# Optimization experiments

Hardware: AMD Instinct MI355X
Metric: run time of the kernel (lower is better)

## Reference

```python
import jax, jax.numpy as jnp
import numpy as np

ANCHOR_SIZES = [64.0, 128.0, 256.0]
ANCHOR_RATIOS = [0.5, 1.0, 2.0]
STD_SCALING = 1.0
RPN_STRIDE = 16
PRE_NMS_TOP_N = 3000
POST_NMS_TOP_N = 300
NMS_IOU_THRES = 0.7


def make_anchors():
    # ratios are sqrt'd as in the original __init__; anchors stored as (w, h)
    rs = [np.sqrt(r) for r in ANCHOR_RATIOS]
    a = [[s * r, s / r] for s in ANCHOR_SIZES for r in rs]
    return np.array(a, dtype=np.float32)  # [A, 2]


def setup_inputs() -> dict:
    key = jax.random.key(0)
    k1, k2 = jax.random.split(key)
    B, A, H, W = 4, 9, 34, 60
    rpn_scores = jax.random.uniform(k1, (B, A, H, W), dtype=jnp.float32)
    rpn_deltas = jax.random.normal(k2, (B, 4 * A, H, W), dtype=jnp.float32)
    input_image = jnp.zeros((B, 3, 544, 960), dtype=jnp.float32)  # only shape is used
    return {"rpn_scores": rpn_scores, "rpn_deltas": rpn_deltas, "input_image": input_image}


def _pairwise_iou(boxes):
    # boxes: [N, 4] in (x1, y1, x2, y2)
    x1, y1, x2, y2 = boxes[:, 0], boxes[:, 1], boxes[:, 2], boxes[:, 3]
    area = (x2 - x1) * (y2 - y1)
    iw = jnp.maximum(jnp.minimum(x2[:, None], x2[None, :]) - jnp.maximum(x1[:, None], x1[None, :]), 0.0)
    ih = jnp.maximum(jnp.minimum(y2[:, None], y2[None, :]) - jnp.maximum(y1[:, None], y1[None, :]), 0.0)
    inter = iw * ih
    union = area[:, None] + area[None, :] - inter
    return inter / jnp.maximum(union, 1e-8)


def _nms_single(boxes, probs):
    # pre-NMS top-N by score, then greedy IoU suppression, then post-NMS top-N (zero-padded)
    scores_k, idx = jax.lax.top_k(probs, PRE_NMS_TOP_N)
    boxes_k = boxes[idx]                                 # [pre_N, 4]
    iou = _pairwise_iou(boxes_k)                         # [pre_N, pre_N]

    def body(active, i):
        keep_i = active[i]
        sup = (iou[i] > NMS_IOU_THRES) & keep_i
        sup = sup.at[i].set(False)
        return active & ~sup, keep_i

    _, keep = jax.lax.scan(body, jnp.ones((PRE_NMS_TOP_N,), bool), jnp.arange(PRE_NMS_TOP_N))
    sel = jnp.where(keep, scores_k, -jnp.inf)
    _, kidx = jax.lax.top_k(sel, POST_NMS_TOP_N)
    valid = keep[kidx]
    return jnp.where(valid[:, None], boxes_k[kidx], 0.0)  # [post_N, 4]


def _forward(rpn_scores, rpn_deltas, input_image):
    B, A, H, W = rpn_scores.shape
    img_h = jnp.float32(input_image.shape[2])
    img_w = jnp.float32(input_image.shape[3])
    # NCHW -> NHWC -> [B,H,W,A,4]; channel layout is anchor-major, coord-minor
    deltas = (rpn_deltas * (1.0 / STD_SCALING)).transpose(0, 2, 3, 1).reshape(B, H, W, A, 4)
    ancs = jnp.asarray(make_anchors())                   # [A, 2] (w, h)
    aw, ah = ancs[:, 0], ancs[:, 1]
    # anchor centers on the RPN grid, at input-image scale
    cx = jnp.broadcast_to(((jnp.arange(W, dtype=jnp.float32) + 0.5) * RPN_STRIDE)[None, :, None], (H, W, A))
    cy = jnp.broadcast_to(((jnp.arange(H, dtype=jnp.float32) + 0.5) * RPN_STRIDE)[:, None, None], (H, W, A))
    tx, ty, tw, th = deltas[..., 0], deltas[..., 1], deltas[..., 2], deltas[..., 3]
    ctr_x = cx + tx * aw
    ctr_y = cy + ty * ah
    w1 = jnp.exp(tw) * aw
    h1 = jnp.exp(th) * ah
    x1 = ctr_x - 0.5 * w1
    y1 = ctr_y - 0.5 * h1
    x2 = x1 + w1
    y2 = y1 + h1
    x1 = jnp.clip(x1, 0.0, img_w - 1.0)
    x2 = jnp.clip(x2, 0.0, img_w - 1.0)
    y1 = jnp.clip(y1, 0.0, img_h - 1.0)
    y2 = jnp.clip(y2, 0.0, img_h - 1.0)
    boxes = jnp.stack([x1, y1, x2, y2], axis=-1)          # [B,H,W,A,4]
    boxes = boxes.transpose(0, 3, 1, 2, 4).reshape(B, -1, 4)  # [B, A*H*W, 4] (matches score layout)
    probs = rpn_scores.reshape(B, -1)
    return jax.vmap(_nms_single)(boxes, probs)            # [B, post_N, 4]


def reference(rpn_scores, rpn_deltas, input_image):
    return _forward(rpn_scores, rpn_deltas, input_image)
```

## Files before the change

kernel.cpp:

```cpp
#include <hip/hip_runtime.h>
#include <stdint.h>

typedef uint32_t u32;
typedef uint64_t u64;

#define NB 4
#define NA 9
#define NH 34
#define NW 60
#define HW (NH*NW)
#define NBOX (NA*HW)
#define PRE_NMS 3000
#define POST_NMS 300
#define NBUCKET 4096
#define SEGCAP 4096
#define NTH 1024
#define PER 18
#define CORNER 512
#define CW 8
#define SUB 16
#define NCH (CORNER/SUB)

__device__ __constant__ float c_aw[9] = {
  45.254833995939045f, 64.0f,  90.50966799187808f,
  90.50966799187808f,  128.0f, 181.01933598375617f,
  181.01933598375617f, 256.0f, 362.03867196751233f };
__device__ __constant__ float c_ah[9] = {
  90.50966799187808f,  64.0f,  45.254833995939045f,
  181.01933598375617f, 128.0f, 90.50966799187808f,
  362.03867196751233f, 256.0f, 181.01933598375617f };

__device__ __forceinline__ u64 readlane64(u64 v, int lane) {
  u32 lo = __builtin_amdgcn_readlane((u32)(v & 0xffffffffull), lane);
  u32 hi = __builtin_amdgcn_readlane((u32)(v >> 32), lane);
  return ((u64)hi << 32) | lo;
}

__device__ __forceinline__ float4 decode_box(const float* __restrict__ dl, int idx) {
  int a = idx / HW;
  int r = idx - a * HW;
  int h = r / NW;
  int w = r - h * NW;
  const float* dp = dl + (4 * a) * HW + r;
  float tx = dp[0];
  float ty = dp[HW];
  float tw = dp[2 * HW];
  float th = dp[3 * HW];
  float aw = c_aw[a], ah = c_ah[a];
  float ctr_x = ((float)w + 0.5f) * 16.0f + tx * aw;
  float ctr_y = ((float)h + 0.5f) * 16.0f + ty * ah;
  float w1 = expf(tw) * aw;
  float h1 = expf(th) * ah;
  float x1 = ctr_x - 0.5f * w1;
  float y1 = ctr_y - 0.5f * h1;
  float x2 = x1 + w1;
  float y2 = y1 + h1;
  x1 = fminf(fmaxf(x1, 0.0f), 959.0f);
  x2 = fminf(fmaxf(x2, 0.0f), 959.0f);
  y1 = fminf(fmaxf(y1, 0.0f), 543.0f);
  y2 = fminf(fmaxf(y2, 0.0f), 543.0f);
  return make_float4(x1, y1, x2, y2);
}

__global__ void __launch_bounds__(NTH)
topk_rank_decode_kernel(const float* __restrict__ scores,
                        const float* __restrict__ deltas,
                        float4* __restrict__ boxes_ws)
{
  __shared__ u32 s_base[NBUCKET];
  __shared__ u32 s_cnt[NBUCKET];
  __shared__ u64 s_keys[SEGCAP];
  __shared__ u32 s_sfx[NTH];

  const int tid = threadIdx.x;
  const int b   = blockIdx.x;
  const float* sc = scores + b * NBOX;

  for (int t = tid; t < NBUCKET; t += NTH) s_cnt[t] = 0;
  __syncthreads();

  for (int m = 0; m < PER; ++m) {
    int i = tid + m * NTH;
    if (i < NBOX) {
      float s = sc[i];
      int bk = (int)(s * (float)NBUCKET);
      bk = bk < 0 ? 0 : (bk > NBUCKET - 1 ? NBUCKET - 1 : bk);
      atomicAdd(&s_cnt[bk], 1u);
    }
  }
  __syncthreads();

  u32 h0 = s_cnt[4*tid], h1 = s_cnt[4*tid+1], h2 = s_cnt[4*tid+2], h3 = s_cnt[4*tid+3];
  s_sfx[tid] = h0 + h1 + h2 + h3;
  __syncthreads();
  for (int d = 1; d < NTH; d <<= 1) {
    u32 v = (tid + d < NTH) ? s_sfx[tid + d] : 0u;
    __syncthreads();
    s_sfx[tid] += v;
    __syncthreads();
  }

  {
    u32 Gn = (tid < NTH - 1) ? s_sfx[tid + 1] : 0u;
    s_base[4*tid+3] = Gn;
    s_base[4*tid+2] = Gn + h3;
    s_base[4*tid+1] = Gn + h3 + h2;
    s_base[4*tid+0] = Gn + h3 + h2 + h1;
  }
  __syncthreads();

  for (int t = tid; t < NBUCKET; t += NTH) s_cnt[t] = 0;
  for (int t = tid; t < SEGCAP; t += NTH) s_keys[t] = 0ull;
  __syncthreads();

  for (int m = 0; m < PER; ++m) {
    int i = tid + m * NTH;
    if (i < NBOX) {
      float s = sc[i];
      int bk = (int)(s * (float)NBUCKET);
      bk = bk < 0 ? 0 : (bk > NBUCKET - 1 ? NBUCKET - 1 : bk);
      u32 base = s_base[bk];
      if (base < PRE_NMS) {
        u32 loc = atomicAdd(&s_cnt[bk], 1u);
        u32 pos = base + loc;
        if (pos < SEGCAP) {
          u64 key = ((u64)__float_as_uint(s) << 32) | (u32)(~(u32)i);
          s_keys[pos] = key;
        }
      }
    }
  }
  __syncthreads();

  const float* dl = deltas + b * (4 * NA * HW);
  for (int m = 0; m < SEGCAP / NTH; ++m) {
    int p = tid + m * NTH;
    u64 key = s_keys[p];
    float s = __uint_as_float((u32)(key >> 32));
    int bk = (int)(s * (float)NBUCKET);
    bk = bk < 0 ? 0 : (bk > NBUCKET - 1 ? NBUCKET - 1 : bk);
    u32 base = s_base[bk];
    u32 cnt  = s_cnt[bk];
    u32 local = 0;
    for (u32 q = base; q < base + cnt; ++q)
      local += (s_keys[q] > key) ? 1u : 0u;
    u32 R = base + local;
    if (key != 0ull && R < PRE_NMS) {
      int idx = (int)(~(u32)key);
      boxes_ws[b * PRE_NMS + R] = decode_box(dl, idx);
    }
  }
}

__global__ void __launch_bounds__(256)
mask_corner_kernel(const float4* __restrict__ boxes_ws, u64* __restrict__ masks2)
{
  const int wq = blockIdx.x;
  const int rh = blockIdx.y;
  const int b  = blockIdx.z;
  const int tid = threadIdx.x;
  __shared__ float4 s_cb[128];
  __shared__ float  s_ca[128];
  if (tid < 128) {
    int j = 128 * wq + tid;
    float4 v = boxes_ws[b * PRE_NMS + j];
    s_cb[tid] = v;
    s_ca[tid] = (v.z - v.x) * (v.w - v.y);
  }
  __syncthreads();
  int row = rh * 256 + tid;
  float4 r = boxes_ws[b * PRE_NMS + row];
  float ra = (r.z - r.x) * (r.w - r.y);
  #pragma unroll
  for (int wl = 0; wl < 2; ++wl) {
    u64 word = 0;
    #pragma unroll
    for (int k = 0; k < 64; ++k) {
      float4 cb = s_cb[wl * 64 + k];
      float iw = fminf(r.z, cb.z) - fmaxf(r.x, cb.x);
      float ih = fminf(r.w, cb.w) - fmaxf(r.y, cb.y);
      iw = fmaxf(iw, 0.0f);
      ih = fmaxf(ih, 0.0f);
      float inter = iw * ih;
      float uni = ra + s_ca[wl * 64 + k] - inter;
      word |= ((u64)(inter > 0.7f * fmaxf(uni, 1e-8f))) << k;
    }
    masks2[((size_t)b * CORNER + row) * CW + (2 * wq + wl)] = word;
  }
}

__global__ void __launch_bounds__(256)
nms_reduce_kernel(const float4* __restrict__ boxes_ws,
                  const u64* __restrict__ masks2,
                  float* __restrict__ out)
{
  const int b = blockIdx.x;
  const int tid = threadIdx.x;
  __shared__ __align__(16) u64 s_corner[CORNER * CW];
  __shared__ u32 s_kept[POST_NMS];
  __shared__ u32 s_nk;

  {
    const ulonglong2* src = (const ulonglong2*)(masks2 + (size_t)b * CORNER * CW);
    ulonglong2* dst = (ulonglong2*)s_corner;
    #pragma unroll
    for (int k = 0; k < (CORNER * CW / 2) / 256; ++k)
      dst[tid + k * 256] = src[tid + k * 256];
  }
  __syncthreads();

  if (tid < 64) {
    const int lane = tid;
    const int wl8 = lane & 7;
    u64 removed = 0ull;
    int nk = 0;
    bool done = false;

    u64 D = (lane < 16) ? s_corner[lane * CW + 0] : 0ull;

    for (int j = 0; j < NCH && !done; ++j) {
      const int base = j * SUB;
      const int w0 = j >> 2;
      const int sh = (j & 3) * 16;
      const int jn = j + 1;
      u64 Dn = (jn < NCH && lane < 16)
                 ? s_corner[(jn * SUB + lane) * CW + (jn >> 2)] : 0ull;
      u64 remw = readlane64(removed, w0);
      u32 a = (u32)((~remw >> sh) & 0xFFFFull);
      u64 supw = 0ull;
      u32 keepm = 0;
      while (a) {
        int k = __ffs(a) - 1;
        a &= a - 1u;
        if (!((supw >> (sh + k)) & 1ull)) {
          keepm |= 1u << k;
          if (lane == 0) s_kept[nk] = (u32)(base + k);
          ++nk;
          if (nk >= POST_NMS) { done = true; break; }
          supw |= readlane64(D, k);
        }
      }
      if (!done) {
        #pragma unroll
        for (int k = 0; k < SUB; ++k) {
          u64 rw = s_corner[(base + k) * CW + wl8];
          if ((keepm >> k) & 1u) removed |= rw;
        }
      }
      D = Dn;
    }

    if (nk < POST_NMS) {
      float4 kb[5];
      float  ka[5];
      #pragma unroll
      for (int s = 0; s < 5; ++s) {
        int t = s * 64 + lane;
        float4 v = make_float4(0.f, 0.f, 0.f, 0.f);
        if (t < nk) v = boxes_ws[b * PRE_NMS + s_kept[t]];
        kb[s] = v;
        ka[s] = (v.z - v.x) * (v.w - v.y);
      }
      for (int i = CORNER; i < PRE_NMS; ++i) {
        if (nk >= POST_NMS) break;
        float4 c = boxes_ws[b * PRE_NMS + i];
        float carea = (c.z - c.x) * (c.w - c.y);
        bool over = false;
        #pragma unroll
        for (int s = 0; s < 5; ++s) {
          if (s * 64 < nk) {
            if (s * 64 + lane < nk) {
              float iw = fminf(kb[s].z, c.z) - fmaxf(kb[s].x, c.x);
              float ih = fminf(kb[s].w, c.w) - fmaxf(kb[s].y, c.y);
              iw = fmaxf(iw, 0.0f);
              ih = fmaxf(ih, 0.0f);
              float inter = iw * ih;
              float uni = ka[s] + carea - inter;
              over = over || (inter > 0.7f * fmaxf(uni, 1e-8f));
            }
          }
        }
        if (__ballot((int)over) == 0ull) {
          int s = nk >> 6, l = nk & 63;
          #pragma unroll
          for (int q = 0; q < 5; ++q)
            if (q == s && lane == l) { kb[q] = c; ka[q] = carea; }
          if (lane == 0) s_kept[nk] = (u32)i;
          ++nk;
        }
      }
    }
    if (lane == 0) s_nk = (u32)nk;
  }
  __syncthreads();

  u32 fnk = s_nk;
  float4* outv = (float4*)out;
  for (int t = tid; t < POST_NMS; t += 256) {
    float4 v = make_float4(0.f, 0.f, 0.f, 0.f);
    if ((u32)t < fnk) v = boxes_ws[b * PRE_NMS + s_kept[t]];
    outv[b * POST_NMS + t] = v;
  }
}

__global__ void __launch_bounds__(NTH)
rpn_proposal_mono(const float* __restrict__ scores,
                  const float* __restrict__ deltas,
                  float* __restrict__ out)
{
  __shared__ __align__(16) char smem[16384 + 32768 + 4096];
  u32* s_hist = (u32*)smem;
  u64* s_cand = (u64*)(smem + 16384);
  u32* s_sfx  = (u32*)(smem + 16384 + 32768);
  float4* s_box = (float4*)smem;
  __shared__ u32 s_kept[POST_NMS];
  __shared__ u32 s_meta[4];

  const int tid = threadIdx.x;
  const int b   = blockIdx.x;
  const float* sc = scores + b * NBOX;

  for (int t = tid; t < NBUCKET; t += NTH) s_hist[t] = 0;
  if (tid < 4) s_meta[tid] = 0;
  __syncthreads();
  for (int m = 0; m < PER; ++m) {
    int i = tid + m * NTH;
    if (i < NBOX) {
      float s = sc[i];
      int bk = (int)(s * (float)NBUCKET);
      bk = bk < 0 ? 0 : (bk > NBUCKET - 1 ? NBUCKET - 1 : bk);
      atomicAdd(&s_hist[bk], 1u);
    }
  }
  __syncthreads();
  {
    u32 g = s_hist[4*tid] + s_hist[4*tid+1] + s_hist[4*tid+2] + s_hist[4*tid+3];
    s_sfx[tid] = g;
  }
  __syncthreads();
  for (int d = 1; d < NTH; d <<= 1) {
    u32 v = (tid + d < NTH) ? s_sfx[tid + d] : 0u;
    __syncthreads();
    s_sfx[tid] += v;
    __syncthreads();
  }
  {
    u32 sg  = s_sfx[tid];
    u32 sgn = (tid < NTH - 1) ? s_sfx[tid + 1] : 0u;
    if (sg >= PRE_NMS && sgn < PRE_NMS) {
      u32 c = sgn;
      for (int t = 4 * tid + 3; t >= 4 * tid; --t) {
        c += s_hist[t];
        if (c >= PRE_NMS) { s_meta[0] = (u32)t; s_meta[1] = c; break; }
      }
    }
  }
  __syncthreads();
  const u32 T = s_meta[0];
  for (int m = 0; m < PER; ++m) {
    int i = tid + m * NTH;
    if (i < NBOX) {
      float s = sc[i];
      int bk = (int)(s * (float)NBUCKET);
      bk = bk < 0 ? 0 : (bk > NBUCKET - 1 ? NBUCKET - 1 : bk);
      if ((u32)bk >= T) {
        u32 pos = atomicAdd(&s_meta[2], 1u);
        if (pos < SEGCAP) {
          u64 key = ((u64)__float_as_uint(s) << 32) | (u32)(~(u32)i);
          s_cand[pos] = key;
        }
      }
    }
  }
  __syncthreads();
  {
    u32 C = s_meta[2]; if (C > SEGCAP) C = SEGCAP;
    for (u32 p = C + tid; p < SEGCAP; p += NTH) s_cand[p] = 0ull;
  }
  for (int kk = 2; kk <= SEGCAP; kk <<= 1) {
    for (int j = kk >> 1; j > 0; j >>= 1) {
      __syncthreads();
      #pragma unroll
      for (int m = 0; m < 2; ++m) {
        int t = tid + m * NTH;
        int i = ((t & ~(j - 1)) << 1) | (t & (j - 1));
        int p = i | j;
        u64 a  = s_cand[i];
        u64 bb = s_cand[p];
        bool desc = (i & kk) == 0;
        bool sw = desc ? (a < bb) : (a > bb);
        if (sw) { s_cand[i] = bb; s_cand[p] = a; }
      }
    }
  }
  __syncthreads();
  const float* dl = deltas + b * (4 * NA * HW);
  float4 bx[3];
  #pragma unroll
  for (int m = 0; m < 3; ++m) {
    int k = tid + m * NTH;
    if (k < PRE_NMS) {
      u64 key = s_cand[k];
      bx[m] = decode_box(dl, (int)(~(u32)key));
    }
  }
  __syncthreads();
  #pragma unroll
  for (int m = 0; m < 3; ++m) {
    int k = tid + m * NTH;
    if (k < PRE_NMS) s_box[k] = bx[m];
  }
  __syncthreads();
  if (tid < 64) {
    const int lane = tid;
    float4 kb[5];
    float  ka[5];
    int nk = 0;
    for (int i = 0; i < PRE_NMS; ++i) {
      if (nk >= POST_NMS) break;
      float4 c = s_box[i];
      float carea = (c.z - c.x) * (c.w - c.y);
      bool over = false;
      #pragma unroll
      for (int s = 0; s < 5; ++s) {
        if (s * 64 < nk) {
          if (s * 64 + lane < nk) {
            float iw = fminf(kb[s].z, c.z) - fmaxf(kb[s].x, c.x);
            float ih = fminf(kb[s].w, c.w) - fmaxf(kb[s].y, c.y);
            iw = fmaxf(iw, 0.0f);
            ih = fmaxf(ih, 0.0f);
            float inter = iw * ih;
            float uni = ka[s] + carea - inter;
            over = over || (inter > 0.7f * fmaxf(uni, 1e-8f));
          }
        }
      }
      if (__ballot((int)over) == 0ull) {
        int s = nk >> 6, l = nk & 63;
        #pragma unroll
        for (int q = 0; q < 5; ++q)
          if (q == s && lane == l) { kb[q] = c; ka[q] = carea; }
        if (lane == 0) s_kept[nk] = (u32)i;
        ++nk;
      }
    }
    if (lane == 0) s_meta[3] = (u32)nk;
  }
  __syncthreads();
  if (tid < POST_NMS) {
    u32 nk = s_meta[3];
    float4 v = make_float4(0.0f, 0.0f, 0.0f, 0.0f);
    if ((u32)tid < nk) v = s_box[s_kept[tid]];
    ((float4*)out)[b * POST_NMS + tid] = v;
  }
}

extern "C" void kernel_launch(void* const* d_in, const int* in_sizes, int n_in,
                              void* d_out, int out_size, void* d_ws, size_t ws_size,
                              hipStream_t stream) {
  const float* scores = (const float*)d_in[0];
  const float* deltas = (const float*)d_in[1];
  (void)in_sizes; (void)n_in; (void)out_size;

  const size_t mask_off   = 196608;
  const size_t mask_bytes = (size_t)NB * CORNER * CW * sizeof(u64);
  const size_t need       = mask_off + mask_bytes;

  if (ws_size >= need) {
    float4* boxes_ws = (float4*)d_ws;
    u64*    masks2   = (u64*)((char*)d_ws + mask_off);
    topk_rank_decode_kernel<<<dim3(NB), dim3(NTH), 0, stream>>>(scores, deltas, boxes_ws);
    mask_corner_kernel<<<dim3(4, 2, NB), dim3(256), 0, stream>>>(boxes_ws, masks2);
    nms_reduce_kernel<<<dim3(NB), dim3(256), 0, stream>>>(boxes_ws, masks2, (float*)d_out);
  } else {
    rpn_proposal_mono<<<dim3(NB), dim3(NTH), 0, stream>>>(scores, deltas, (float*)d_out);
  }
}
```

Measured before the change: 150.1 us.

## Expand precomputed IoU mask to 1536 candidates with register-resident row-chain NMS

The precomputed suppression bitmask grows from the top 512 to the top 1536 candidates (24 words per row), and the corner mask kernel now launches more blocks, one 64-column word each. The reduce kernel becomes a single wavefront. For each 64-box chunk it ORs each lane's mask row against the accumulated keep masks held in registers, uses a ballot to find unsuppressed boxes, resolves the intra-chunk greedy order with readlane, and prefetches the next chunk's rows from global memory. This moves more of the greedy scan off the slow serial per-candidate IoU fallback. The cost is a larger mask computation and workspace, plus heavy register use.

```diff
diff --git a/kernel.cpp b/kernel.cpp
--- a/kernel.cpp
+++ b/kernel.cpp
@@ -16,10 +16,9 @@
 #define SEGCAP 4096
 #define NTH 1024
 #define PER 18
-#define CORNER 512
-#define CW 8
-#define SUB 16
-#define NCH (CORNER/SUB)
+#define NCAND 1536
+#define MW 24
+#define NCHK 24
 
 __device__ __constant__ float c_aw[9] = {
   45.254833995939045f, 64.0f,  90.50966799187808f,
@@ -156,149 +155,177 @@
 mask_corner_kernel(const float4* __restrict__ boxes_ws, u64* __restrict__ masks2)
 {
   const int wq = blockIdx.x;
-  const int rh = blockIdx.y;
+  const int rb = blockIdx.y;
   const int b  = blockIdx.z;
   const int tid = threadIdx.x;
-  __shared__ float4 s_cb[128];
-  __shared__ float  s_ca[128];
-  if (tid < 128) {
-    int j = 128 * wq + tid;
+  __shared__ float4 s_cb[64];
+  __shared__ float  s_ca[64];
+  if (tid < 64) {
+    int j = wq * 64 + tid;
     float4 v = boxes_ws[b * PRE_NMS + j];
     s_cb[tid] = v;
     s_ca[tid] = (v.z - v.x) * (v.w - v.y);
   }
   __syncthreads();
-  int row = rh * 256 + tid;
+  int row = rb * 256 + tid;
   float4 r = boxes_ws[b * PRE_NMS + row];
   float ra = (r.z - r.x) * (r.w - r.y);
+  u64 word = 0;
   #pragma unroll
-  for (int wl = 0; wl < 2; ++wl) {
-    u64 word = 0;
-    #pragma unroll
-    for (int k = 0; k < 64; ++k) {
-      float4 cb = s_cb[wl * 64 + k];
-      float iw = fminf(r.z, cb.z) - fmaxf(r.x, cb.x);
-      float ih = fminf(r.w, cb.w) - fmaxf(r.y, cb.y);
-      iw = fmaxf(iw, 0.0f);
-      ih = fmaxf(ih, 0.0f);
-      float inter = iw * ih;
-      float uni = ra + s_ca[wl * 64 + k] - inter;
-      word |= ((u64)(inter > 0.7f * fmaxf(uni, 1e-8f))) << k;
-    }
-    masks2[((size_t)b * CORNER + row) * CW + (2 * wq + wl)] = word;
-  }
-}
-
-__global__ void __launch_bounds__(256)
+  for (int k = 0; k < 64; ++k) {
+    float4 cb = s_cb[k];
+    float iw = fminf(r.z, cb.z) - fmaxf(r.x, cb.x);
+    float ih = fminf(r.w, cb.w) - fmaxf(r.y, cb.y);
+    iw = fmaxf(iw, 0.0f);
+    ih = fmaxf(ih, 0.0f);
+    float inter = iw * ih;
+    float uni = ra + s_ca[k] - inter;
+    word |= ((u64)(inter > 0.7f * fmaxf(uni, 1e-8f))) << k;
+  }
+  masks2[((size_t)b * NCAND + row) * MW + wq] = word;
+}
+
+__global__ void __launch_bounds__(64)
 nms_reduce_kernel(const float4* __restrict__ boxes_ws,
                   const u64* __restrict__ masks2,
                   float* __restrict__ out)
 {
   const int b = blockIdx.x;
-  const int tid = threadIdx.x;
-  __shared__ __align__(16) u64 s_corner[CORNER * CW];
+  const int lane = threadIdx.x;
   __shared__ u32 s_kept[POST_NMS];
-  __shared__ u32 s_nk;
-
-  {
-    const ulonglong2* src = (const ulonglong2*)(masks2 + (size_t)b * CORNER * CW);
-    ulonglong2* dst = (ulonglong2*)s_corner;
+
+  const u64* mrow = masks2 + (size_t)b * NCAND * MW;
+  int nk = 0;
+  bool done = false;
+
+  ulonglong2 cur0, cur1, cur2, cur3, cur4, cur5, cur6, cur7, cur8, cur9, cur10, cur11;
+  ulonglong2 nxt0, nxt1, nxt2, nxt3, nxt4, nxt5, nxt6, nxt7, nxt8, nxt9, nxt10, nxt11;
+  ulonglong2 km0, km1, km2, km3, km4, km5, km6, km7, km8, km9, km10, km11;
+  km0 = km1 = km2 = km3 = km4 = km5 = km6 = km7 = km8 = km9 = km10 = km11
+      = make_ulonglong2(0ull, 0ull);
+
+#define LOADCUR(C) { const ulonglong2* p_ = (const ulonglong2*)mrow + ((size_t)((C)*64 + lane)) * (MW/2); \
+  cur0=p_[0]; cur1=p_[1]; cur2=p_[2]; cur3=p_[3]; cur4=p_[4]; cur5=p_[5]; \
+  cur6=p_[6]; cur7=p_[7]; cur8=p_[8]; cur9=p_[9]; cur10=p_[10]; cur11=p_[11]; }
+#define PREF(C) { const ulonglong2* p_ = (const ulonglong2*)mrow + ((size_t)((C)*64 + lane)) * (MW/2); \
+  nxt0=p_[0]; nxt1=p_[1]; nxt2=p_[2]; nxt3=p_[3]; nxt4=p_[4]; nxt5=p_[5]; \
+  nxt6=p_[6]; nxt7=p_[7]; nxt8=p_[8]; nxt9=p_[9]; nxt10=p_[10]; nxt11=p_[11]; }
+#define ROLL { cur0=nxt0; cur1=nxt1; cur2=nxt2; cur3=nxt3; cur4=nxt4; cur5=nxt5; \
+  cur6=nxt6; cur7=nxt7; cur8=nxt8; cur9=nxt9; cur10=nxt10; cur11=nxt11; }
+#define DO_CHUNK(C, DW, KM) {                                            \
+    u64 sA_ = (cur0.x & km0.x) | (cur0.y & km0.y)                        \
+            | (cur1.x & km1.x) | (cur1.y & km1.y)                        \
+            | (cur2.x & km2.x) | (cur2.y & km2.y)                        \
+            | (cur3.x & km3.x) | (cur3.y & km3.y)                        \
+            | (cur4.x & km4.x) | (cur4.y & km4.y)                        \
+            | (cur5.x & km5.x) | (cur5.y & km5.y)                        \
+            | (cur6.x & km6.x) | (cur6.y & km6.y)                        \
+            | (cur7.x & km7.x) | (cur7.y & km7.y)                        \
+            | (cur8.x & km8.x) | (cur8.y & km8.y)                        \
+            | (cur9.x & km9.x) | (cur9.y & km9.y)                        \
+            | (cur10.x & km10.x) | (cur10.y & km10.y)                    \
+            | (cur11.x & km11.x) | (cur11.y & km11.y);                   \
+    u64 a_ = __ballot(sA_ == 0ull);                                      \
+    u64 supw_ = 0ull, keepm_ = 0ull;                                     \
+    while (a_) {                                                         \
+      int k_ = __ffsll((unsigned long long)a_) - 1;                      \
+      a_ &= a_ - 1ull;                                                   \
+      if (!((supw_ >> k_) & 1ull)) {                                     \
+        keepm_ |= 1ull << k_;                                            \
+        ++nk;                                                            \
+        if (nk >= POST_NMS) break;                                       \
+        supw_ |= readlane64(DW, k_);                                     \
+      }                                                                  \
+    }                                                                    \
+    if (lane == 0) {                                                     \
+      u64 km_ = keepm_;                                                  \
+      int c2_ = nk - __popcll((unsigned long long)keepm_);               \
+      while (km_) {                                                      \
+        int k_ = __ffsll((unsigned long long)km_) - 1;                   \
+        km_ &= km_ - 1ull;                                               \
+        s_kept[c2_++] = (u32)((C) * 64 + k_);                            \
+      }                                                                  \
+    }                                                                    \
+    KM |= keepm_;                                                        \
+    done = (nk >= POST_NMS);                                             \
+  }
+
+  LOADCUR(0); PREF(1);
+  DO_CHUNK( 0, cur0.x,  km0.x ); if (done) goto chain_done; ROLL; PREF(2);
+  DO_CHUNK( 1, cur0.y,  km0.y ); if (done) goto chain_done; ROLL; PREF(3);
+  DO_CHUNK( 2, cur1.x,  km1.x ); if (done) goto chain_done; ROLL; PREF(4);
+  DO_CHUNK( 3, cur1.y,  km1.y ); if (done) goto chain_done; ROLL; PREF(5);
+  DO_CHUNK( 4, cur2.x,  km2.x ); if (done) goto chain_done; ROLL; PREF(6);
+  DO_CHUNK( 5, cur2.y,  km2.y ); if (done) goto chain_done; ROLL; PREF(7);
+  DO_CHUNK( 6, cur3.x,  km3.x ); if (done) goto chain_done; ROLL; PREF(8);
+  DO_CHUNK( 7, cur3.y,  km3.y ); if (done) goto chain_done; ROLL; PREF(9);
+  DO_CHUNK( 8, cur4.x,  km4.x ); if (done) goto chain_done; ROLL; PREF(10);
+  DO_CHUNK( 9, cur4.y,  km4.y ); if (done) goto chain_done; ROLL; PREF(11);
+  DO_CHUNK(10, cur5.x,  km5.x ); if (done) goto chain_done; ROLL; PREF(12);
+  DO_CHUNK(11, cur5.y,  km5.y ); if (done) goto chain_done; ROLL; PREF(13);
+  DO_CHUNK(12, cur6.x,  km6.x ); if (done) goto chain_done; ROLL; PREF(14);
+  DO_CHUNK(13, cur6.y,  km6.y ); if (done) goto chain_done; ROLL; PREF(15);
+  DO_CHUNK(14, cur7.x,  km7.x ); if (done) goto chain_done; ROLL; PREF(16);
+  DO_CHUNK(15, cur7.y,  km7.y ); if (done) goto chain_done; ROLL; PREF(17);
+  DO_CHUNK(16, cur8.x,  km8.x ); if (done) goto chain_done; ROLL; PREF(18);
+  DO_CHUNK(17, cur8.y,  km8.y ); if (done) goto chain_done; ROLL; PREF(19);
+  DO_CHUNK(18, cur9.x,  km9.x ); if (done) goto chain_done; ROLL; PREF(20);
+  DO_CHUNK(19, cur9.y,  km9.y ); if (done) goto chain_done; ROLL; PREF(21);
+  DO_CHUNK(20, cur10.x, km10.x); if (done) goto chain_done; ROLL; PREF(22);
+  DO_CHUNK(21, cur10.y, km10.y); if (done) goto chain_done; ROLL; PREF(23);
+  DO_CHUNK(22, cur11.x, km11.x); if (done) goto chain_done; ROLL;
+  DO_CHUNK(23, cur11.y, km11.y);
+chain_done: ;
+#undef DO_CHUNK
+#undef ROLL
+#undef PREF
+#undef LOADCUR
+
+  if (nk < POST_NMS) {
+    float4 kb[5];
+    float  ka[5];
     #pragma unroll
-    for (int k = 0; k < (CORNER * CW / 2) / 256; ++k)
-      dst[tid + k * 256] = src[tid + k * 256];
-  }
-  __syncthreads();
-
-  if (tid < 64) {
-    const int lane = tid;
-    const int wl8 = lane & 7;
-    u64 removed = 0ull;
-    int nk = 0;
-    bool done = false;
-
-    u64 D = (lane < 16) ? s_corner[lane * CW + 0] : 0ull;
-
-    for (int j = 0; j < NCH && !done; ++j) {
-      const int base = j * SUB;
-      const int w0 = j >> 2;
-      const int sh = (j & 3) * 16;
-      const int jn = j + 1;
-      u64 Dn = (jn < NCH && lane < 16)
-                 ? s_corner[(jn * SUB + lane) * CW + (jn >> 2)] : 0ull;
-      u64 remw = readlane64(removed, w0);
-      u32 a = (u32)((~remw >> sh) & 0xFFFFull);
-      u64 supw = 0ull;
-      u32 keepm = 0;
-      while (a) {
-        int k = __ffs(a) - 1;
-        a &= a - 1u;
-        if (!((supw >> (sh + k)) & 1ull)) {
-          keepm |= 1u << k;
-          if (lane == 0) s_kept[nk] = (u32)(base + k);
-          ++nk;
-          if (nk >= POST_NMS) { done = true; break; }
-          supw |= readlane64(D, k);
-        }
-      }
-      if (!done) {
-        #pragma unroll
-        for (int k = 0; k < SUB; ++k) {
-          u64 rw = s_corner[(base + k) * CW + wl8];
-          if ((keepm >> k) & 1u) removed |= rw;
-        }
-      }
-      D = Dn;
-    }
-
-    if (nk < POST_NMS) {
-      float4 kb[5];
-      float  ka[5];
+    for (int s = 0; s < 5; ++s) {
+      int t = s * 64 + lane;
+      float4 v = make_float4(0.f, 0.f, 0.f, 0.f);
+      if (t < nk) v = boxes_ws[b * PRE_NMS + s_kept[t]];
+      kb[s] = v;
+      ka[s] = (v.z - v.x) * (v.w - v.y);
+    }
+    for (int i = NCAND; i < PRE_NMS; ++i) {
+      if (nk >= POST_NMS) break;
+      float4 c = boxes_ws[b * PRE_NMS + i];
+      float carea = (c.z - c.x) * (c.w - c.y);
+      bool over = false;
       #pragma unroll
       for (int s = 0; s < 5; ++s) {
-        int t = s * 64 + lane;
-        float4 v = make_float4(0.f, 0.f, 0.f, 0.f);
-        if (t < nk) v = boxes_ws[b * PRE_NMS + s_kept[t]];
-        kb[s] = v;
-        ka[s] = (v.z - v.x) * (v.w - v.y);
-      }
-      for (int i = CORNER; i < PRE_NMS; ++i) {
-        if (nk >= POST_NMS) break;
-        float4 c = boxes_ws[b * PRE_NMS + i];
-        float carea = (c.z - c.x) * (c.w - c.y);
-        bool over = false;
-        #pragma unroll
-        for (int s = 0; s < 5; ++s) {
-          if (s * 64 < nk) {
-            if (s * 64 + lane < nk) {
-              float iw = fminf(kb[s].z, c.z) - fmaxf(kb[s].x, c.x);
-              float ih = fminf(kb[s].w, c.w) - fmaxf(kb[s].y, c.y);
-              iw = fmaxf(iw, 0.0f);
-              ih = fmaxf(ih, 0.0f);
-              float inter = iw * ih;
-              float uni = ka[s] + carea - inter;
-              over = over || (inter > 0.7f * fmaxf(uni, 1e-8f));
-            }
+        if (s * 64 < nk) {
+          if (s * 64 + lane < nk) {
+            float iw = fminf(kb[s].z, c.z) - fmaxf(kb[s].x, c.x);
+            float ih = fminf(kb[s].w, c.w) - fmaxf(kb[s].y, c.y);
+            iw = fmaxf(iw, 0.0f);
+            ih = fmaxf(ih, 0.0f);
+            float inter = iw * ih;
+            float uni = ka[s] + carea - inter;
+            over = over || (inter > 0.7f * fmaxf(uni, 1e-8f));
           }
         }
-        if (__ballot((int)over) == 0ull) {
-          int s = nk >> 6, l = nk & 63;
-          #pragma unroll
-          for (int q = 0; q < 5; ++q)
-            if (q == s && lane == l) { kb[q] = c; ka[q] = carea; }
-          if (lane == 0) s_kept[nk] = (u32)i;
-          ++nk;
-        }
-      }
-    }
-    if (lane == 0) s_nk = (u32)nk;
-  }
-  __syncthreads();
-
-  u32 fnk = s_nk;
+      }
+      if (__ballot((int)over) == 0ull) {
+        int s = nk >> 6, l = nk & 63;
+        #pragma unroll
+        for (int q = 0; q < 5; ++q)
+          if (q == s && lane == l) { kb[q] = c; ka[q] = carea; }
+        if (lane == 0) s_kept[nk] = (u32)i;
+        ++nk;
+      }
+    }
+  }
+
   float4* outv = (float4*)out;
-  for (int t = tid; t < POST_NMS; t += 256) {
+  for (int t = lane; t < POST_NMS; t += 64) {
     float4 v = make_float4(0.f, 0.f, 0.f, 0.f);
-    if ((u32)t < fnk) v = boxes_ws[b * PRE_NMS + s_kept[t]];
+    if (t < nk) v = boxes_ws[b * PRE_NMS + s_kept[t]];
     outv[b * POST_NMS + t] = v;
   }
 }
@@ -463,15 +490,15 @@
   (void)in_sizes; (void)n_in; (void)out_size;
 
   const size_t mask_off   = 196608;
-  const size_t mask_bytes = (size_t)NB * CORNER * CW * sizeof(u64);
+  const size_t mask_bytes = (size_t)NB * NCAND * MW * sizeof(u64);
   const size_t need       = mask_off + mask_bytes;
 
   if (ws_size >= need) {
     float4* boxes_ws = (float4*)d_ws;
     u64*    masks2   = (u64*)((char*)d_ws + mask_off);
     topk_rank_decode_kernel<<<dim3(NB), dim3(NTH), 0, stream>>>(scores, deltas, boxes_ws);
-    mask_corner_kernel<<<dim3(4, 2, NB), dim3(256), 0, stream>>>(boxes_ws, masks2);
-    nms_reduce_kernel<<<dim3(NB), dim3(256), 0, stream>>>(boxes_ws, masks2, (float*)d_out);
+    mask_corner_kernel<<<dim3(MW, NCAND / 256, NB), dim3(256), 0, stream>>>(boxes_ws, masks2);
+    nms_reduce_kernel<<<dim3(NB), dim3(64), 0, stream>>>(boxes_ws, masks2, (float*)d_out);
   } else {
     rpn_proposal_mono<<<dim3(NB), dim3(NTH), 0, stream>>>(scores, deltas, (float*)d_out);
   }
```

After: 143.5 us. 4.4% less time.

## Enlarge precomputed IoU mask region and double-buffer chunked NMS reduction

Applied to the files above, without the earlier changes.

The precomputed IoU bitmask region grows from a 512x512 corner to 1088 rows by 17 words. The greedy NMS now walks 64-box chunks: one wavefront prefetches the next chunk's mask rows into a double-buffered LDS area while the other wavefront resolves the current chunk against a kept-bitmask. The hierarchical suffix scan in the top-k kernel is also replaced by a single-wave register and shuffle scan, removing about 20 block barriers. This cuts the slow serial fallback loop over boxes past the corner, at the cost of a larger mask kernel launch and per-chunk block barriers.

```diff
diff --git a/kernel.cpp b/kernel.cpp
--- a/kernel.cpp
+++ b/kernel.cpp
@@ -16,10 +16,9 @@
 #define SEGCAP 4096
 #define NTH 1024
 #define PER 18
-#define CORNER 512
-#define CW 8
-#define SUB 16
-#define NCH (CORNER/SUB)
+#define NCAND 1088
+#define MWc 17
+#define NCHK 17
 
 __device__ __constant__ float c_aw[9] = {
   45.254833995939045f, 64.0f,  90.50966799187808f,
@@ -93,12 +92,33 @@
   u32 h0 = s_cnt[4*tid], h1 = s_cnt[4*tid+1], h2 = s_cnt[4*tid+2], h3 = s_cnt[4*tid+3];
   s_sfx[tid] = h0 + h1 + h2 + h3;
   __syncthreads();
-  for (int d = 1; d < NTH; d <<= 1) {
-    u32 v = (tid + d < NTH) ? s_sfx[tid + d] : 0u;
-    __syncthreads();
-    s_sfx[tid] += v;
-    __syncthreads();
-  }
+  if (tid < 64) {
+    const int l = tid;
+    u32 v0,v1,v2,v3,v4,v5,v6,v7,v8,v9,v10,v11,v12,v13,v14,v15;
+    {
+      const u32* p = &s_sfx[l * 16];
+      v0=p[0]; v1=p[1]; v2=p[2]; v3=p[3]; v4=p[4]; v5=p[5]; v6=p[6]; v7=p[7];
+      v8=p[8]; v9=p[9]; v10=p[10]; v11=p[11]; v12=p[12]; v13=p[13]; v14=p[14]; v15=p[15];
+    }
+    v14+=v15; v13+=v14; v12+=v13; v11+=v12; v10+=v11; v9+=v10; v8+=v9; v7+=v8;
+    v6+=v7; v5+=v6; v4+=v5; v3+=v4; v2+=v3; v1+=v2; v0+=v1;
+    u32 tot = v0;
+    u32 inc = tot;
+    #pragma unroll
+    for (int off = 1; off < 64; off <<= 1) {
+      u32 x = (u32)__shfl_down((int)inc, off, 64);
+      if (l + off < 64) inc += x;
+    }
+    u32 exc = inc - tot;
+    {
+      u32* p = &s_sfx[l * 16];
+      p[0]=v0+exc; p[1]=v1+exc; p[2]=v2+exc; p[3]=v3+exc;
+      p[4]=v4+exc; p[5]=v5+exc; p[6]=v6+exc; p[7]=v7+exc;
+      p[8]=v8+exc; p[9]=v9+exc; p[10]=v10+exc; p[11]=v11+exc;
+      p[12]=v12+exc; p[13]=v13+exc; p[14]=v14+exc; p[15]=v15+exc;
+    }
+  }
+  __syncthreads();
 
   {
     u32 Gn = (tid < NTH - 1) ? s_sfx[tid + 1] : 0u;
@@ -156,100 +176,102 @@
 mask_corner_kernel(const float4* __restrict__ boxes_ws, u64* __restrict__ masks2)
 {
   const int wq = blockIdx.x;
-  const int rh = blockIdx.y;
+  const int rb = blockIdx.y;
   const int b  = blockIdx.z;
   const int tid = threadIdx.x;
-  __shared__ float4 s_cb[128];
-  __shared__ float  s_ca[128];
-  if (tid < 128) {
-    int j = 128 * wq + tid;
+  __shared__ float4 s_cb[64];
+  __shared__ float  s_ca[64];
+  if (tid < 64) {
+    int j = wq * 64 + tid;
     float4 v = boxes_ws[b * PRE_NMS + j];
     s_cb[tid] = v;
     s_ca[tid] = (v.z - v.x) * (v.w - v.y);
   }
   __syncthreads();
-  int row = rh * 256 + tid;
-  float4 r = boxes_ws[b * PRE_NMS + row];
-  float ra = (r.z - r.x) * (r.w - r.y);
-  #pragma unroll
-  for (int wl = 0; wl < 2; ++wl) {
+  int row = rb * 256 + tid;
+  if (row < NCAND) {
+    float4 r = boxes_ws[b * PRE_NMS + row];
+    float ra = (r.z - r.x) * (r.w - r.y);
     u64 word = 0;
     #pragma unroll
     for (int k = 0; k < 64; ++k) {
-      float4 cb = s_cb[wl * 64 + k];
+      float4 cb = s_cb[k];
       float iw = fminf(r.z, cb.z) - fmaxf(r.x, cb.x);
       float ih = fminf(r.w, cb.w) - fmaxf(r.y, cb.y);
       iw = fmaxf(iw, 0.0f);
       ih = fmaxf(ih, 0.0f);
       float inter = iw * ih;
-      float uni = ra + s_ca[wl * 64 + k] - inter;
+      float uni = ra + s_ca[k] - inter;
       word |= ((u64)(inter > 0.7f * fmaxf(uni, 1e-8f))) << k;
     }
-    masks2[((size_t)b * CORNER + row) * CW + (2 * wq + wl)] = word;
-  }
-}
-
-__global__ void __launch_bounds__(256)
+    masks2[((size_t)b * NCAND + row) * MWc + wq] = word;
+  }
+}
+
+__global__ void __launch_bounds__(128)
 nms_reduce_kernel(const float4* __restrict__ boxes_ws,
                   const u64* __restrict__ masks2,
                   float* __restrict__ out)
 {
   const int b = blockIdx.x;
   const int tid = threadIdx.x;
-  __shared__ __align__(16) u64 s_corner[CORNER * CW];
+  const int wv = tid >> 6;
+  const int lane = tid & 63;
+
+  __shared__ __align__(16) u64 s_buf[2][64 * MWc];
+  __shared__ u64 s_bm[MWc];
   __shared__ u32 s_kept[POST_NMS];
   __shared__ u32 s_nk;
 
-  {
-    const ulonglong2* src = (const ulonglong2*)(masks2 + (size_t)b * CORNER * CW);
-    ulonglong2* dst = (ulonglong2*)s_corner;
+  const u64* mbase = masks2 + (size_t)b * NCAND * MWc;
+
+  if (wv == 1) {
     #pragma unroll
-    for (int k = 0; k < (CORNER * CW / 2) / 256; ++k)
-      dst[tid + k * 256] = src[tid + k * 256];
-  }
-  __syncthreads();
-
-  if (tid < 64) {
-    const int lane = tid;
-    const int wl8 = lane & 7;
-    u64 removed = 0ull;
-    int nk = 0;
-    bool done = false;
-
-    u64 D = (lane < 16) ? s_corner[lane * CW + 0] : 0ull;
-
-    for (int j = 0; j < NCH && !done; ++j) {
-      const int base = j * SUB;
-      const int w0 = j >> 2;
-      const int sh = (j & 3) * 16;
-      const int jn = j + 1;
-      u64 Dn = (jn < NCH && lane < 16)
-                 ? s_corner[(jn * SUB + lane) * CW + (jn >> 2)] : 0ull;
-      u64 remw = readlane64(removed, w0);
-      u32 a = (u32)((~remw >> sh) & 0xFFFFull);
-      u64 supw = 0ull;
-      u32 keepm = 0;
+    for (int w = 0; w < MWc; ++w)
+      s_buf[0][lane + w * 64] = mbase[lane + w * 64];
+  } else if (lane < MWc) {
+    s_bm[lane] = 0ull;
+  }
+  __syncthreads();
+
+  int nk = 0;
+  bool fin = false;
+
+  for (int chunk = 0; chunk < NCHK; ++chunk) {
+    if (wv == 1) {
+      if (chunk + 1 < NCHK) {
+        const u64* src = mbase + (size_t)(chunk + 1) * 64 * MWc;
+        u64* dst = s_buf[(chunk + 1) & 1];
+        #pragma unroll
+        for (int w = 0; w < MWc; ++w)
+          dst[lane + w * 64] = src[lane + w * 64];
+      }
+    } else if (!fin) {
+      const u64* row = &s_buf[chunk & 1][lane * MWc];
+      u64 s = 0ull;
+      #pragma unroll
+      for (int w = 0; w < MWc; ++w)
+        s |= row[w] & s_bm[w];
+      u64 D = row[chunk];
+      u64 a = __ballot(s == 0ull);
+      u64 supw = 0ull, keepm = 0ull;
       while (a) {
-        int k = __ffs(a) - 1;
-        a &= a - 1u;
-        if (!((supw >> (sh + k)) & 1ull)) {
-          keepm |= 1u << k;
-          if (lane == 0) s_kept[nk] = (u32)(base + k);
+        int k = __ffsll((unsigned long long)a) - 1;
+        a &= a - 1ull;
+        if (!((supw >> k) & 1ull)) {
+          keepm |= 1ull << k;
+          if (lane == 0) s_kept[nk] = (u32)(chunk * 64 + k);
           ++nk;
-          if (nk >= POST_NMS) { done = true; break; }
+          if (nk >= POST_NMS) { fin = true; break; }
           supw |= readlane64(D, k);
         }
       }
-      if (!done) {
-        #pragma unroll
-        for (int k = 0; k < SUB; ++k) {
-          u64 rw = s_corner[(base + k) * CW + wl8];
-          if ((keepm >> k) & 1u) removed |= rw;
-        }
-      }
-      D = Dn;
-    }
-
+      if (lane == 0) s_bm[chunk] = keepm;
+    }
+    __syncthreads();
+  }
+
+  if (wv == 0) {
     if (nk < POST_NMS) {
       float4 kb[5];
       float  ka[5];
@@ -261,7 +283,7 @@
         kb[s] = v;
         ka[s] = (v.z - v.x) * (v.w - v.y);
       }
-      for (int i = CORNER; i < PRE_NMS; ++i) {
+      for (int i = NCAND; i < PRE_NMS; ++i) {
         if (nk >= POST_NMS) break;
         float4 c = boxes_ws[b * PRE_NMS + i];
         float carea = (c.z - c.x) * (c.w - c.y);
@@ -296,7 +318,7 @@
 
   u32 fnk = s_nk;
   float4* outv = (float4*)out;
-  for (int t = tid; t < POST_NMS; t += 256) {
+  for (int t = tid; t < POST_NMS; t += 128) {
     float4 v = make_float4(0.f, 0.f, 0.f, 0.f);
     if ((u32)t < fnk) v = boxes_ws[b * PRE_NMS + s_kept[t]];
     outv[b * POST_NMS + t] = v;
@@ -463,15 +485,15 @@
   (void)in_sizes; (void)n_in; (void)out_size;
 
   const size_t mask_off   = 196608;
-  const size_t mask_bytes = (size_t)NB * CORNER * CW * sizeof(u64);
+  const size_t mask_bytes = (size_t)NB * NCAND * MWc * sizeof(u64);
   const size_t need       = mask_off + mask_bytes;
 
   if (ws_size >= need) {
     float4* boxes_ws = (float4*)d_ws;
     u64*    masks2   = (u64*)((char*)d_ws + mask_off);
     topk_rank_decode_kernel<<<dim3(NB), dim3(NTH), 0, stream>>>(scores, deltas, boxes_ws);
-    mask_corner_kernel<<<dim3(4, 2, NB), dim3(256), 0, stream>>>(boxes_ws, masks2);
-    nms_reduce_kernel<<<dim3(NB), dim3(256), 0, stream>>>(boxes_ws, masks2, (float*)d_out);
+    mask_corner_kernel<<<dim3(MWc, (NCAND + 255) / 256, NB), dim3(256), 0, stream>>>(boxes_ws, masks2);
+    nms_reduce_kernel<<<dim3(NB), dim3(128), 0, stream>>>(boxes_ws, masks2, (float*)d_out);
   } else {
     rpn_proposal_mono<<<dim3(NB), dim3(NTH), 0, stream>>>(scores, deltas, (float*)d_out);
   }
```

Result: slower. 161.7 us (+7.7%).
